# Performance work log

Measured on AMD Instinct MI355X. Metric: run time of the kernel, lower is better.

Reference implementation:

```python
import jax, jax.numpy as jnp
import numpy as np
import math

MAX_DEGREE = 8  # n_harmonics = (MAX_DEGREE+1)**2 = 81


def _real_sph_harm_all(theta, phi, L):
    """Real part of scipy's sph_harm(m, l, phi, theta) for all (l, m),
    l in [0, L], m in [-l, l], stacked on the last axis (81 terms for L=8).

    Uses the stable associated-Legendre recurrence (with Condon-Shortley
    phase, matching scipy) instead of a per-term CPU loop.
    """
    x = jnp.cos(theta)
    s = jnp.sin(theta)  # sin(theta) >= 0 since theta in [0, pi]

    # P[(l, m)] = associated Legendre P_l^m(cos theta), 0 <= m <= l <= L
    P = {}
    for m in range(L + 1):
        if m == 0:
            Pmm = jnp.ones_like(x)
        else:
            # P_m^m = -(2m-1) * sin(theta) * P_{m-1}^{m-1}  (Condon-Shortley)
            Pmm = -(2 * m - 1) * s * P[(m - 1, m - 1)]
        P[(m, m)] = Pmm
        if m + 1 <= L:
            P[(m + 1, m)] = (2 * m + 1) * x * Pmm
        for l in range(m + 2, L + 1):
            P[(l, m)] = ((2 * l - 1) * x * P[(l - 1, m)]
                         - (l + m - 1) * P[(l - 2, m)]) / (l - m)

    ys = []
    for l in range(L + 1):
        for m in range(-l, l + 1):
            am = abs(m)
            norm = math.sqrt((2 * l + 1) / (4.0 * math.pi)
                             * math.factorial(l - am) / math.factorial(l + am))
            # Re(Y_l^m) = N * P_l^{|m|}(cos th) * cos(|m| phi); for m<0 multiply
            # by (-1)^{|m|} since Y_l^{-m} = (-1)^m conj(Y_l^m) (scipy convention).
            Y = norm * P[(l, am)] * jnp.cos(am * phi)
            if m < 0:
                Y = Y * ((-1.0) ** am)
            ys.append(Y)
    return jnp.stack(ys, axis=-1)  # [batch, channels, (L+1)^2]


def setup_inputs() -> dict:
    key = jax.random.key(0)
    k1, k2 = jax.random.split(key)
    positions = jax.random.normal(k1, (32, 1024, 3), dtype=jnp.float32)
    harmonics_weights = jax.random.normal(k2, (81, 2048), dtype=jnp.float32)
    return {"positions": positions, "harmonics_weights": harmonics_weights}


def reference(positions, harmonics_weights):
    # normalize to unit sphere
    r = jnp.linalg.norm(positions, axis=-1, keepdims=True)
    pos = positions / (r + 1e-8)
    theta = jnp.arccos(jnp.clip(pos[..., 2], -1.0, 1.0))  # polar angle
    phi = jnp.arctan2(pos[..., 1], pos[..., 0])           # azimuth
    harmonics = _real_sph_harm_all(theta, phi, MAX_DEGREE)  # [B, C, 81]
    return jnp.matmul(harmonics, harmonics_weights)         # [B, C, 2048]
```

## Files before the change

### kernel.cpp

```cpp
#include <hip/hip_runtime.h>


typedef __attribute__((ext_vector_type(8))) short bf16x8;
typedef __attribute__((ext_vector_type(4))) float f32x4;

#define BM 128
#define BN 128
#define LDA 104
#define KPAD 96

constexpr double PI_D = 3.14159265358979323846;
constexpr double csqrt_c(double v) {
  if (v <= 0.0) return 0.0;
  double g = v < 1.0 ? 1.0 : v;
  for (int i = 0; i < 100; ++i) g = 0.5 * (g + v / g);
  return g;
}
struct Norms { float c[81]; };
constexpr Norms make_norms() {
  Norms n{};
  for (int l = 0; l <= 8; ++l)
    for (int m = -l; m <= l; ++m) {
      int am = m < 0 ? -m : m;
      double fr = 1.0;
      for (int i = l - am + 1; i <= l + am; ++i) fr *= (double)i;
      double v = csqrt_c((2.0 * l + 1.0) / (4.0 * PI_D) / fr);
      if (m < 0 && (am & 1)) v = -v;
      n.c[l * l + l + m] = (float)v;
    }
  return n;
}
constexpr Norms NORMS = make_norms();

__device__ __forceinline__ unsigned f2bf(float f) {
  unsigned u = __float_as_uint(f);
  return (u + 0x7fffu + ((u >> 16) & 1u)) >> 16;
}

__global__ __launch_bounds__(256)
void wt_convert_kernel(const float* __restrict__ W, unsigned short* __restrict__ WT, int nch) {
  const int t = blockIdx.x * 256 + threadIdx.x;
  if (t >= nch * 12) return;
  const int kg = t / nch;
  const int c  = t - kg * nch;
  unsigned short v[8];
#pragma unroll
  for (int j = 0; j < 8; ++j) {
    const int k = kg * 8 + j;
    v[j] = (k < 81) ? (unsigned short)f2bf(W[(size_t)k * nch + c]) : (unsigned short)0;
  }
  unsigned* dst = reinterpret_cast<unsigned*>(WT + (size_t)c * KPAD + kg * 8);
#pragma unroll
  for (int j = 0; j < 4; ++j)
    dst[j] = (unsigned)v[2 * j] | ((unsigned)v[2 * j + 1] << 16);
}

__global__ __launch_bounds__(256)
void sph_mfma_kernel(const float* __restrict__ pos,
                     const unsigned short* __restrict__ WT,
                     float* __restrict__ out, int nch)
{
  __shared__ unsigned short H[BM * LDA];
  const int tid  = threadIdx.x;
  const int lane = tid & 63;
  const int wid  = tid >> 6;
  const int wc   = wid >> 1, wp = wid & 1;
  const int l15  = lane & 15, l4 = lane >> 4;
  const int mblk = blockIdx.y, nblk = blockIdx.x;

  if (tid < BM) {
    const int gp = mblk * BM + tid;
    const float px = pos[gp * 3 + 0];
    const float py = pos[gp * 3 + 1];
    const float pz = pos[gp * 3 + 2];
    const float r   = sqrtf(px * px + py * py + pz * pz);
    const float inv = 1.0f / (r + 1e-8f);
    const float xn = px * inv, yn = py * inv, zn = pz * inv;
    const float x = fminf(1.0f, fmaxf(-1.0f, zn));
    const float s = sqrtf(fmaxf(0.0f, 1.0f - x * x));
    const float rho = sqrtf(xn * xn + yn * yn);
    const float c1  = rho > 0.0f ? xn / rho : 1.0f;

    float cm[9];
    cm[0] = 1.0f; cm[1] = c1;
#pragma unroll
    for (int m = 2; m <= 8; ++m) cm[m] = 2.0f * c1 * cm[m - 1] - cm[m - 2];

    float P[9][9];
#pragma unroll
    for (int m = 0; m <= 8; ++m) {
      if (m == 0) P[0][0] = 1.0f;
      else        P[m][m] = -(float)(2 * m - 1) * s * P[m - 1][m - 1];
      if (m + 1 <= 8) P[m + 1][m] = (float)(2 * m + 1) * x * P[m][m];
#pragma unroll
      for (int l = m + 2; l <= 8; ++l)
        P[l][m] = ((float)(2 * l - 1) * x * P[l - 1][m]
                   - (float)(l + m - 1) * P[l - 2][m]) / (float)(l - m);
    }

    float y[KPAD];
#pragma unroll
    for (int l = 0; l <= 8; ++l)
#pragma unroll
      for (int m = -l; m <= l; ++m) {
        const int am  = m < 0 ? -m : m;
        const int idx = l * l + l + m;
        y[idx] = NORMS.c[idx] * P[l][am] * cm[am];
      }
#pragma unroll
    for (int i = 81; i < KPAD; ++i) y[i] = 0.0f;

    unsigned* hrow = reinterpret_cast<unsigned*>(&H[tid * LDA]);
#pragma unroll
    for (int i = 0; i < KPAD / 2; ++i)
      hrow[i] = f2bf(y[2 * i]) | (f2bf(y[2 * i + 1]) << 16);
  }

  bf16x8 wfrag[3][4];
  const unsigned short* wt_base =
      WT + (size_t)(nblk * BN + wc * 64 + l15) * KPAD + l4 * 8;
#pragma unroll
  for (int kk = 0; kk < 3; ++kk)
#pragma unroll
    for (int cmr = 0; cmr < 4; ++cmr)
      wfrag[kk][cmr] = *reinterpret_cast<const bf16x8*>(
          wt_base + (size_t)cmr * 16 * KPAD + kk * 32);

  __syncthreads();

  f32x4 acc[4][4] = {};
#pragma unroll
  for (int kk = 0; kk < 3; ++kk) {
    bf16x8 hfrag[4];
#pragma unroll
    for (int pn = 0; pn < 4; ++pn)
      hfrag[pn] = *reinterpret_cast<const bf16x8*>(
          &H[(wp * 64 + pn * 16 + l15) * LDA + kk * 32 + l4 * 8]);
#pragma unroll
    for (int cmr = 0; cmr < 4; ++cmr)
#pragma unroll
      for (int pn = 0; pn < 4; ++pn)
        acc[cmr][pn] = __builtin_amdgcn_mfma_f32_16x16x32_bf16(
            wfrag[kk][cmr], hfrag[pn], acc[cmr][pn], 0, 0, 0);
  }

  const size_t ch0 = (size_t)nblk * BN + wc * 64 + l4 * 4;
  const size_t pt0 = (size_t)mblk * BM + wp * 64 + l15;
#pragma unroll
  for (int pn = 0; pn < 4; ++pn) {
    float* orow = out + (pt0 + pn * 16) * nch + ch0;
#pragma unroll
    for (int cmr = 0; cmr < 4; ++cmr)
      *reinterpret_cast<f32x4*>(orow + cmr * 16) = acc[cmr][pn];
  }
}

extern "C" void kernel_launch(void* const* d_in, const int* in_sizes, int n_in,
                              void* d_out, int out_size, void* d_ws, size_t ws_size,
                              hipStream_t stream) {
  const float* pos = (const float*)d_in[0];
  const float* W   = (const float*)d_in[1];
  float*       out = (float*)d_out;
  const int npts = in_sizes[0] / 3;
  const int nch  = in_sizes[1] / 81;

  unsigned short* WT = (unsigned short*)d_ws;
  const int cvt_threads = nch * 12;
  wt_convert_kernel<<<(cvt_threads + 255) / 256, 256, 0, stream>>>(W, WT, nch);
  dim3 grid(nch / BN, npts / BM);
  sph_mfma_kernel<<<grid, 256, 0, stream>>>(pos, WT, out, nch);
}
```

Baseline: 61.22 us.

## Stage output tile through LDS for coalesced stores, stream harmonics directly to LDS

The accumulator tile is now written to shared memory in two halves and read back so each thread stores contiguous 16-byte chunks along full 128-channel rows, replacing the strided per-lane f32x4 global stores. The harmonic computation writes bf16 values straight into the LDS row as they are produced, so the 9x9 P array and the 96-entry y array no longer sit in registers. Weight fragments are loaded per k-step instead of all up front, which also lowers register use. The cost is extra barriers and an LDS round trip, and the shared buffer is reused between H and C.

```diff
diff --git a/kernel.cpp b/kernel.cpp
--- a/kernel.cpp
+++ b/kernel.cpp
@@ -8,6 +8,7 @@
 #define BN 128
 #define LDA 104
 #define KPAD 96
+#define LDCC 132
 
 constexpr double PI_D = 3.14159265358979323846;
 constexpr double csqrt_c(double v) {
@@ -60,7 +61,10 @@
                      const unsigned short* __restrict__ WT,
                      float* __restrict__ out, int nch)
 {
-  __shared__ unsigned short H[BM * LDA];
+  __shared__ __align__(16) char smem[64 * LDCC * 4];
+  unsigned short* H = reinterpret_cast<unsigned short*>(smem);
+  float*          C = reinterpret_cast<float*>(smem);
+
   const int tid  = threadIdx.x;
   const int lane = tid & 63;
   const int wid  = tid >> 6;
@@ -86,72 +90,90 @@
 #pragma unroll
     for (int m = 2; m <= 8; ++m) cm[m] = 2.0f * c1 * cm[m - 1] - cm[m - 2];
 
-    float P[9][9];
+    unsigned short* hrow = &H[tid * LDA];
+    float Pmm_prev = 1.0f;
 #pragma unroll
     for (int m = 0; m <= 8; ++m) {
-      if (m == 0) P[0][0] = 1.0f;
-      else        P[m][m] = -(float)(2 * m - 1) * s * P[m - 1][m - 1];
-      if (m + 1 <= 8) P[m + 1][m] = (float)(2 * m + 1) * x * P[m][m];
-#pragma unroll
-      for (int l = m + 2; l <= 8; ++l)
-        P[l][m] = ((float)(2 * l - 1) * x * P[l - 1][m]
-                   - (float)(l + m - 1) * P[l - 2][m]) / (float)(l - m);
-    }
-
-    float y[KPAD];
-#pragma unroll
-    for (int l = 0; l <= 8; ++l)
-#pragma unroll
-      for (int m = -l; m <= l; ++m) {
-        const int am  = m < 0 ? -m : m;
-        const int idx = l * l + l + m;
-        y[idx] = NORMS.c[idx] * P[l][am] * cm[am];
+      const float Pmm = (m == 0) ? 1.0f : -(float)(2 * m - 1) * s * Pmm_prev;
+      Pmm_prev = Pmm;
+      {
+        const float base = Pmm * cm[m];
+        hrow[m * m + 2 * m] = (unsigned short)f2bf(NORMS.c[m * m + 2 * m] * base);
+        if (m > 0)
+          hrow[m * m] = (unsigned short)f2bf(NORMS.c[m * m] * base);
+      }
+      float Pl2 = Pmm, Pl1 = 0.0f;
+      if (m + 1 <= 8) {
+        Pl1 = (float)(2 * m + 1) * x * Pmm;
+        const int l = m + 1;
+        const float base = Pl1 * cm[m];
+        hrow[l * l + l + m] = (unsigned short)f2bf(NORMS.c[l * l + l + m] * base);
+        if (m > 0)
+          hrow[l * l + l - m] = (unsigned short)f2bf(NORMS.c[l * l + l - m] * base);
       }
 #pragma unroll
-    for (int i = 81; i < KPAD; ++i) y[i] = 0.0f;
-
-    unsigned* hrow = reinterpret_cast<unsigned*>(&H[tid * LDA]);
+      for (int l = m + 2; l <= 8; ++l) {
+        const float Pl = ((float)(2 * l - 1) * x * Pl1
+                          - (float)(l + m - 1) * Pl2) * (1.0f / (float)(l - m));
+        Pl2 = Pl1; Pl1 = Pl;
+        const float base = Pl * cm[m];
+        hrow[l * l + l + m] = (unsigned short)f2bf(NORMS.c[l * l + l + m] * base);
+        if (m > 0)
+          hrow[l * l + l - m] = (unsigned short)f2bf(NORMS.c[l * l + l - m] * base);
+      }
+    }
 #pragma unroll
-    for (int i = 0; i < KPAD / 2; ++i)
-      hrow[i] = f2bf(y[2 * i]) | (f2bf(y[2 * i + 1]) << 16);
+    for (int i = 81; i < KPAD; ++i) hrow[i] = 0;
   }
-
-  bf16x8 wfrag[3][4];
-  const unsigned short* wt_base =
-      WT + (size_t)(nblk * BN + wc * 64 + l15) * KPAD + l4 * 8;
-#pragma unroll
-  for (int kk = 0; kk < 3; ++kk)
-#pragma unroll
-    for (int cmr = 0; cmr < 4; ++cmr)
-      wfrag[kk][cmr] = *reinterpret_cast<const bf16x8*>(
-          wt_base + (size_t)cmr * 16 * KPAD + kk * 32);
 
   __syncthreads();
 
+  const unsigned short* wt_base =
+      WT + (size_t)(nblk * BN + wc * 64 + l15) * KPAD + l4 * 8;
   f32x4 acc[4][4] = {};
 #pragma unroll
   for (int kk = 0; kk < 3; ++kk) {
-    bf16x8 hfrag[4];
+    bf16x8 wfrag[4], hfrag[4];
 #pragma unroll
-    for (int pn = 0; pn < 4; ++pn)
-      hfrag[pn] = *reinterpret_cast<const bf16x8*>(
-          &H[(wp * 64 + pn * 16 + l15) * LDA + kk * 32 + l4 * 8]);
+    for (int i = 0; i < 4; ++i)
+      wfrag[i] = *reinterpret_cast<const bf16x8*>(
+          wt_base + (size_t)i * 16 * KPAD + kk * 32);
+#pragma unroll
+    for (int i = 0; i < 4; ++i)
+      hfrag[i] = *reinterpret_cast<const bf16x8*>(
+          &H[(wp * 64 + i * 16 + l15) * LDA + kk * 32 + l4 * 8]);
 #pragma unroll
     for (int cmr = 0; cmr < 4; ++cmr)
 #pragma unroll
       for (int pn = 0; pn < 4; ++pn)
         acc[cmr][pn] = __builtin_amdgcn_mfma_f32_16x16x32_bf16(
-            wfrag[kk][cmr], hfrag[pn], acc[cmr][pn], 0, 0, 0);
+            wfrag[cmr], hfrag[pn], acc[cmr][pn], 0, 0, 0);
   }
 
-  const size_t ch0 = (size_t)nblk * BN + wc * 64 + l4 * 4;
-  const size_t pt0 = (size_t)mblk * BM + wp * 64 + l15;
+  __syncthreads();
+
+  const size_t obase = (size_t)(mblk * BM) * nch + (size_t)nblk * BN;
 #pragma unroll
-  for (int pn = 0; pn < 4; ++pn) {
-    float* orow = out + (pt0 + pn * 16) * nch + ch0;
+  for (int h = 0; h < 2; ++h) {
 #pragma unroll
-    for (int cmr = 0; cmr < 4; ++cmr)
-      *reinterpret_cast<f32x4*>(orow + cmr * 16) = acc[cmr][pn];
+    for (int q = 0; q < 2; ++q) {
+      const int lr = wp * 32 + q * 16 + l15;
+#pragma unroll
+      for (int cmr = 0; cmr < 4; ++cmr)
+        *reinterpret_cast<f32x4*>(&C[lr * LDCC + wc * 64 + cmr * 16 + l4 * 4]) =
+            acc[cmr][2 * h + q];
+    }
+    __syncthreads();
+#pragma unroll
+    for (int it = 0; it < 8; ++it) {
+      const int f  = it * 1024 + tid * 4;
+      const int lr = f >> 7;
+      const int cc = f & 127;
+      const int gr = (lr >> 5) * 64 + h * 32 + (lr & 31);
+      const f32x4 v = *reinterpret_cast<const f32x4*>(&C[lr * LDCC + cc]);
+      *reinterpret_cast<f32x4*>(out + obase + (size_t)gr * nch + cc) = v;
+    }
+    if (h == 0) __syncthreads();
   }
 }
 
@@ -165,8 +187,7 @@
   const int nch  = in_sizes[1] / 81;
 
   unsigned short* WT = (unsigned short*)d_ws;
-  const int cvt_threads = nch * 12;
-  wt_convert_kernel<<<(cvt_threads + 255) / 256, 256, 0, stream>>>(W, WT, nch);
+  wt_convert_kernel<<<(nch * 12 + 255) / 256, 256, 0, stream>>>(W, WT, nch);
   dim3 grid(nch / BN, npts / BM);
   sph_mfma_kernel<<<grid, 256, 0, stream>>>(pos, WT, out, nch);
 }
```

Result: faster. 56.73 us (-7.3%).
